# Kernel tuning notes

Hardware: AMD Instinct MI355X
Metric: run time of the kernel (lower is better)

Reference implementation:

```python
import jax, jax.numpy as jnp
import numpy as np

B, NC, CN, K, DN = 2, 256, 256, 16, 64
G, HM, HS, HMOD, MOD_OUT = 8, 128, 128, 64, 5


def setup_inputs() -> dict:
    rng = np.random.default_rng(0)
    # per-neuron top-K neighbors within cell, excluding self, sorted (matches torch buffer build)
    scores = rng.random((NC, CN, CN)).astype(np.float32)
    ii = np.arange(CN)
    scores[:, ii, ii] = -np.inf
    conn = np.argpartition(-scores, K, axis=-1)[..., :K]
    conn = np.sort(conn, axis=-1).astype(np.int32)  # [NC, CN, K]

    key = jax.random.key(0)
    ks = jax.random.split(key, 12)
    n = lambda k, s, sc=1.0: jax.random.normal(k, s, jnp.float32) * sc
    return {
        'h': n(ks[0], (B, NC, CN, DN), 0.01),
        'w_conn': n(ks[1], (B, NC, CN, K), 0.1),
        'cell_context': n(ks[2], (B, NC, DN), 0.1),
        'neuron_id': n(ks[3], (NC, CN, DN), 0.02),
        'msg_w1': n(ks[4], (G, HM, 3 * DN), 0.05), 'msg_b1': jnp.zeros((G, HM)),
        'msg_w2': n(ks[5], (G, DN, HM), 0.005), 'msg_b2': jnp.zeros((G, DN)),
        'state_w1': n(ks[6], (G, HS, 3 * DN), 0.05), 'state_b1': jnp.zeros((G, HS)),
        'state_w2': n(ks[7], (G, DN, HS), 0.005), 'state_b2': jnp.zeros((G, DN)),
        'mod_w1': n(ks[8], (NC, 2 * DN, HMOD), 0.05), 'mod_b1': jnp.zeros((NC, HMOD)),
        'mod_w2': n(ks[9], (NC, HMOD, MOD_OUT), 0.0005), 'mod_b2': jnp.zeros((NC, MOD_OUT)),
        'conn_idx': jnp.asarray(conn),
        'cell_to_group': (jnp.arange(NC) % G).astype(jnp.int32),
    }


def reference(h, w_conn, cell_context, neuron_id,
              msg_w1, msg_b1, msg_w2, msg_b2,
              state_w1, state_b1, state_w2, state_b2,
              mod_w1, mod_b1, mod_w2, mod_b2,
              conn_idx, cell_to_group):
    nc = h.shape[1]
    cell_ix = jnp.arange(nc)[:, None, None]
    # gather K-neighbor states per neuron: [B, NC, CN, K, DN]
    nb = jax.vmap(lambda hb: hb[cell_ix, conn_idx])(h)
    # connection-weighted aggregation
    agg = jnp.einsum('bnck,bnckd->bncd', w_conn, nb)

    g = cell_to_group  # [NC]
    # grouped message MLP (2-layer), per-cell weights gathered from group table
    mfeat = jnp.concatenate([h, agg, jnp.broadcast_to(neuron_id[None], h.shape)], axis=-1)
    mh = jax.nn.gelu(jnp.einsum('bncf,nhf->bnch', mfeat, msg_w1[g]) + msg_b1[g][None, :, None, :])
    msg = jnp.einsum('bnch,ndh->bncd', mh, msg_w2[g]) + msg_b2[g][None, :, None, :]

    # grouped state MLP, residual update on h
    ctx = jnp.broadcast_to(cell_context[:, :, None, :], h.shape)
    sfeat = jnp.concatenate([h, msg, ctx], axis=-1)
    sh = jax.nn.gelu(jnp.einsum('bncf,nhf->bnch', sfeat, state_w1[g]) + state_b1[g][None, :, None, :])
    h_new = h + jnp.einsum('bnch,ndh->bncd', sh, state_w2[g]) + state_b2[g][None, :, None, :]

    # per-cell modulation MLP on pooled stats (h_mean || msg_mean)
    pooled = jnp.concatenate([h_new.mean(axis=2), msg.mean(axis=2)], axis=-1)  # [B, NC, 2DN]
    ph = jax.nn.gelu(jnp.einsum('bnf,nfh->bnh', pooled, mod_w1) + mod_b1[None])
    mod = jnp.einsum('bnh,nho->bno', ph, mod_w2) + mod_b2[None]
    return h_new, msg, mod
```

## Files before the change

### kernel.cpp

```cpp
#include <hip/hip_runtime.h>

#define NC_  256
#define CN_  256
#define K_   16
#define DN_  64
#define G_   8
#define HM_  128
#define F3_  192

typedef unsigned short u16;
typedef short v8s __attribute__((ext_vector_type(8)));
typedef float v4f __attribute__((ext_vector_type(4)));


__device__ __forceinline__ u16 f2b(float f) {
    unsigned v; __builtin_memcpy(&v, &f, 4);
    v = v + 0x7fffu + ((v >> 16) & 1u);
    return (u16)(v >> 16);
}
__device__ __forceinline__ v8s cvt8(const float* p) {
    float4 a = *(const float4*)p, b = *(const float4*)(p + 4);
    v8s r;
    r[0] = (short)f2b(a.x); r[1] = (short)f2b(a.y); r[2] = (short)f2b(a.z); r[3] = (short)f2b(a.w);
    r[4] = (short)f2b(b.x); r[5] = (short)f2b(b.y); r[6] = (short)f2b(b.z); r[7] = (short)f2b(b.w);
    return r;
}
__device__ __forceinline__ float gelu_t(float x) {
    float u = x * x;
    float t = 1.5957691216057308f * x * __builtin_fmaf(0.044715f, u, 1.0f);
    float e = __expf(-t);
    return x * __builtin_amdgcn_rcpf(1.0f + e);
}

__global__ __launch_bounds__(256) void cvt_w(
    const float* __restrict__ mw1, const float* __restrict__ mw2,
    const float* __restrict__ sw1, const float* __restrict__ sw2,
    u16* __restrict__ dst)
{
    int e = (blockIdx.x * 256 + threadIdx.x) * 4;
    const float* s; int off;
    if      (e < 196608) { s = mw1; off = e; }
    else if (e < 262144) { s = mw2; off = e - 196608; }
    else if (e < 458752) { s = sw1; off = e - 262144; }
    else                 { s = sw2; off = e - 458752; }
    float4 v = *(const float4*)(s + off);
    ushort4 o4;
    o4.x = f2b(v.x); o4.y = f2b(v.y); o4.z = f2b(v.z); o4.w = f2b(v.w);
    *(ushort4*)(dst + e) = o4;
}

__global__ __launch_bounds__(256) void gth(
    const float* __restrict__ h, const float* __restrict__ wconn,
    const int* __restrict__ conn, float* __restrict__ outf)
{
    const int p     = blockIdx.x;
    const int bnc   = (p & 7) * 64 + (p >> 6);
    const int chunk = (p >> 3) & 7;
    const int wave  = threadIdx.x >> 6, lane = threadIdx.x & 63;
    const int r0    = chunk * 32 + wave * 8;
    const int n     = bnc & 255;
    const size_t hb = (size_t)bnc * 16384;
    const float* __restrict__ hp = h + hb;
    float* aggo = outf + (size_t)8388608 + hb;
    const int*   __restrict__ cp = conn  + n * 4096 + r0 * 16;
    const float* __restrict__ wp = wconn + (size_t)bnc * 4096 + (size_t)r0 * 16;
    int   ivA = cp[lane],      ivB = cp[64 + lane];
    float wvA = wp[lane],      wvB = wp[64 + lane];
#pragma unroll
    for (int i = 0; i < 8; ++i) {
        int   iv = (i < 4) ? ivA : ivB;
        float wv = (i < 4) ? wvA : wvB;
        float a0 = 0.0f, a1 = 0.0f;
#pragma unroll
        for (int k = 0; k < 16; k += 2) {
            const int l0 = (i & 3) * 16 + k;
            int   i0 = __builtin_amdgcn_readlane(iv, l0);
            int   i1 = __builtin_amdgcn_readlane(iv, l0 + 1);
            float w0 = __int_as_float(__builtin_amdgcn_readlane(__float_as_int(wv), l0));
            float w1 = __int_as_float(__builtin_amdgcn_readlane(__float_as_int(wv), l0 + 1));
            a0 = __builtin_fmaf(w0, hp[i0 * 64 + lane], a0);
            a1 = __builtin_fmaf(w1, hp[i1 * 64 + lane], a1);
        }
        aggo[(size_t)(r0 + i) * 64 + lane] = a0 + a1;
    }
}

__global__ __launch_bounds__(64, 3) void mg_main(
    const float* __restrict__ h,    const float* __restrict__ ctx,
    const float* __restrict__ nid,
    const u16* __restrict__ mw1b,   const float* __restrict__ mb1,
    const u16* __restrict__ mw2b,   const float* __restrict__ mb2,
    const u16* __restrict__ sw1b,   const float* __restrict__ sb1,
    const u16* __restrict__ sw2b,   const float* __restrict__ sb2,
    const int* __restrict__ c2g,
    float* __restrict__ outf,       float* __restrict__ partial)
{
    const int p     = blockIdx.x;
    const int bnc   = (p & 7) * 64 + (p >> 6);
    const int chunk = (p >> 3) & 7;
    const int r0    = chunk * 32;
    const int n     = bnc & 255;
    const int g     = c2g[n];
    const int lane  = threadIdx.x;
    const int q     = lane >> 4, ln = lane & 15;

    __shared__ u16 mh[32 * 138];
    __shared__ u16 am[32 * 74];

    const size_t hbase = (size_t)bnc * 16384;
    const size_t nbase = (size_t)n   * 16384;
    float* oH = outf + hbase;
    float* oM = outf + (size_t)8388608 + hbase;
    const size_t pbase = (size_t)(bnc * 8 + chunk) * 128;

    v8s hfr[2][2], gfr[2][2], nfr[2][2];
#pragma unroll
    for (int mi = 0; mi < 2; ++mi) {
        int c = r0 + mi * 16 + ln;
        hfr[mi][0] = cvt8(h   + hbase + (size_t)c * 64 +  0 + q * 8);
        hfr[mi][1] = cvt8(h   + hbase + (size_t)c * 64 + 32 + q * 8);
        gfr[mi][0] = cvt8(oM  + (size_t)c * 64 +  0 + q * 8);
        gfr[mi][1] = cvt8(oM  + (size_t)c * 64 + 32 + q * 8);
        nfr[mi][0] = cvt8(nid + nbase + (size_t)c * 64 +  0 + q * 8);
        nfr[mi][1] = cvt8(nid + nbase + (size_t)c * 64 + 32 + q * 8);
    }

    {
        v8s afr0[6] = {hfr[0][0], hfr[0][1], gfr[0][0], gfr[0][1], nfr[0][0], nfr[0][1]};
        v8s afr1[6] = {hfr[1][0], hfr[1][1], gfr[1][0], gfr[1][1], nfr[1][0], nfr[1][1]};
        float b1v[8];
#pragma unroll
        for (int nt = 0; nt < 8; ++nt) b1v[nt] = mb1[g * HM_ + nt * 16 + ln];
        const u16* w1g = mw1b + (size_t)g * HM_ * F3_;
#pragma unroll
        for (int nt = 0; nt < 8; ++nt) {
            v4f acc0 = {0,0,0,0}, acc1 = {0,0,0,0};
#pragma unroll
            for (int ks = 0; ks < 6; ++ks) {
                v8s bf = *(const v8s*)(w1g + (nt * 16 + ln) * F3_ + ks * 32 + q * 8);
                acc0 = __builtin_amdgcn_mfma_f32_16x16x32_bf16(afr0[ks], bf, acc0, 0, 0, 0);
                acc1 = __builtin_amdgcn_mfma_f32_16x16x32_bf16(afr1[ks], bf, acc1, 0, 0, 0);
            }
            int c0 = q * 4, c1 = 16 + q * 4;
#pragma unroll
            for (int r = 0; r < 4; ++r) {
                mh[(c0 + r) * 138 + nt * 16 + ln] = f2b(gelu_t(acc0[r] + b1v[nt]));
                mh[(c1 + r) * 138 + nt * 16 + ln] = f2b(gelu_t(acc1[r] + b1v[nt]));
            }
        }
    }

    {
        v8s afr[2][4];
#pragma unroll
        for (int mi = 0; mi < 2; ++mi) {
            int c = mi * 16 + ln;
#pragma unroll
            for (int ks = 0; ks < 4; ++ks)
                afr[mi][ks] = *(const v8s*)(mh + c * 138 + ks * 32 + q * 8);
        }
        const u16* w2g = mw2b + (size_t)g * DN_ * HM_;
        float mpart[4];
#pragma unroll
        for (int nt = 0; nt < 4; ++nt) {
            float bb = mb2[g * DN_ + nt * 16 + ln];
            v4f acc[2] = {{0,0,0,0},{0,0,0,0}};
#pragma unroll
            for (int ks = 0; ks < 4; ++ks) {
                v8s bf = *(const v8s*)(w2g + (nt * 16 + ln) * HM_ + ks * 32 + q * 8);
#pragma unroll
                for (int mi = 0; mi < 2; ++mi)
                    acc[mi] = __builtin_amdgcn_mfma_f32_16x16x32_bf16(afr[mi][ks], bf, acc[mi], 0, 0, 0);
            }
            float ms = 0.0f;
            int d = nt * 16 + ln;
#pragma unroll
            for (int mi = 0; mi < 2; ++mi) {
                int c = mi * 16 + q * 4;
#pragma unroll
                for (int r = 0; r < 4; ++r) {
                    float mv = acc[mi][r] + bb;
                    am[(c + r) * 74 + d] = f2b(mv);
                    oM[(size_t)(r0 + c + r) * 64 + d] = mv;
                    ms += mv;
                }
            }
            mpart[nt] = ms;
        }
#pragma unroll
        for (int nt = 0; nt < 4; ++nt) {
            float v = mpart[nt];
            v += __shfl_xor(v, 16);
            v += __shfl_xor(v, 32);
            if (q == 0) partial[pbase + 64 + nt * 16 + ln] = v * (1.0f / 256.0f);
        }
    }

    {
        v8s cfr0 = cvt8(ctx + (size_t)bnc * DN_ +  0 + q * 8);
        v8s cfr1 = cvt8(ctx + (size_t)bnc * DN_ + 32 + q * 8);
        v8s afr[2][4];
#pragma unroll
        for (int mi = 0; mi < 2; ++mi) {
            int c = mi * 16 + ln;
            afr[mi][0] = hfr[mi][0];
            afr[mi][1] = hfr[mi][1];
            afr[mi][2] = *(const v8s*)(am + c * 74 +  0 + q * 8);
            afr[mi][3] = *(const v8s*)(am + c * 74 + 32 + q * 8);
        }
        float b1v[8];
#pragma unroll
        for (int nt = 0; nt < 8; ++nt) b1v[nt] = sb1[g * HM_ + nt * 16 + ln];
        const u16* w1g = sw1b + (size_t)g * HM_ * F3_;
#pragma unroll
        for (int nt = 0; nt < 8; ++nt) {
            v4f acc[2] = {{0,0,0,0},{0,0,0,0}};
#pragma unroll
            for (int ks = 0; ks < 4; ++ks) {
                v8s bf = *(const v8s*)(w1g + (nt * 16 + ln) * F3_ + ks * 32 + q * 8);
#pragma unroll
                for (int mi = 0; mi < 2; ++mi)
                    acc[mi] = __builtin_amdgcn_mfma_f32_16x16x32_bf16(afr[mi][ks], bf, acc[mi], 0, 0, 0);
            }
#pragma unroll
            for (int ks = 4; ks < 6; ++ks) {
                v8s bf = *(const v8s*)(w1g + (nt * 16 + ln) * F3_ + ks * 32 + q * 8);
                v8s aa = (ks == 4) ? cfr0 : cfr1;
#pragma unroll
                for (int mi = 0; mi < 2; ++mi)
                    acc[mi] = __builtin_amdgcn_mfma_f32_16x16x32_bf16(aa, bf, acc[mi], 0, 0, 0);
            }
#pragma unroll
            for (int mi = 0; mi < 2; ++mi) {
                int c = mi * 16 + q * 4;
#pragma unroll
                for (int r = 0; r < 4; ++r)
                    mh[(c + r) * 138 + nt * 16 + ln] = f2b(gelu_t(acc[mi][r] + b1v[nt]));
            }
        }
    }

    {
        v8s afr[2][4];
#pragma unroll
        for (int mi = 0; mi < 2; ++mi) {
            int c = mi * 16 + ln;
#pragma unroll
            for (int ks = 0; ks < 4; ++ks)
                afr[mi][ks] = *(const v8s*)(mh + c * 138 + ks * 32 + q * 8);
        }
        const u16* w2g = sw2b + (size_t)g * DN_ * HM_;
        float hpart[4];
#pragma unroll
        for (int nt = 0; nt < 4; ++nt) {
            float bb = sb2[g * DN_ + nt * 16 + ln];
            v4f acc[2] = {{0,0,0,0},{0,0,0,0}};
#pragma unroll
            for (int ks = 0; ks < 4; ++ks) {
                v8s bf = *(const v8s*)(w2g + (nt * 16 + ln) * HM_ + ks * 32 + q * 8);
#pragma unroll
                for (int mi = 0; mi < 2; ++mi)
                    acc[mi] = __builtin_amdgcn_mfma_f32_16x16x32_bf16(afr[mi][ks], bf, acc[mi], 0, 0, 0);
            }
            float hs = 0.0f;
            int d = nt * 16 + ln;
#pragma unroll
            for (int mi = 0; mi < 2; ++mi) {
                int c = mi * 16 + q * 4;
#pragma unroll
                for (int r = 0; r < 4; ++r) {
                    float hv = h[hbase + (size_t)(r0 + c + r) * 64 + d];
                    float hn = hv + acc[mi][r] + bb;
                    oH[(size_t)(r0 + c + r) * 64 + d] = hn;
                    hs += hn;
                }
            }
            hpart[nt] = hs;
        }
#pragma unroll
        for (int nt = 0; nt < 4; ++nt) {
            float v = hpart[nt];
            v += __shfl_xor(v, 16);
            v += __shfl_xor(v, 32);
            if (q == 0) partial[pbase + nt * 16 + ln] = v * (1.0f / 256.0f);
        }
    }
}

__global__ __launch_bounds__(256) void mg_mod(
    const float* __restrict__ w1, const float* __restrict__ b1,
    const float* __restrict__ w2, const float* __restrict__ b2,
    const float* __restrict__ partial, float* __restrict__ outf)
{
    __shared__ float pool[128];
    __shared__ float ph4[4][64];
    const int bnc = blockIdx.x, n = bnc & 255, t = threadIdx.x;
    if (t < 128) {
        const float* pp = partial + (size_t)bnc * 1024 + t;
        float s = 0.0f;
#pragma unroll
        for (int j = 0; j < 8; ++j) s += pp[j * 128];
        pool[t] = s;
    }
    __syncthreads();
    {
        const int col = t & 63, fh = t >> 6;
        const float* w1p = w1 + ((size_t)n * 128 + fh * 32) * 64 + col;
        float acc = 0.0f;
#pragma unroll
        for (int i = 0; i < 32; ++i)
            acc = __builtin_fmaf(pool[fh * 32 + i], w1p[(size_t)i * 64], acc);
        ph4[fh][col] = acc;
    }
    __syncthreads();
    if (t < 64) {
        float a  = ph4[0][t] + ph4[1][t] + ph4[2][t] + ph4[3][t] + b1[n * 64 + t];
        float ph = gelu_t(a);
        float part5[5];
#pragma unroll
        for (int o = 0; o < 5; ++o) part5[o] = ph * w2[((size_t)n * 64 + t) * 5 + o];
#pragma unroll
        for (int off = 32; off > 0; off >>= 1)
#pragma unroll
            for (int o = 0; o < 5; ++o) part5[o] += __shfl_down(part5[o], off);
        if (t == 0) {
#pragma unroll
            for (int o = 0; o < 5; ++o)
                outf[(size_t)16777216 + bnc * 5 + o] = part5[o] + b2[n * 5 + o];
        }
    }
}

extern "C" void kernel_launch(void* const* d_in, const int* in_sizes, int n_in,
                              void* d_out, int out_size, void* d_ws, size_t ws_size,
                              hipStream_t stream) {
    const float* h     = (const float*)d_in[0];
    const float* wconn = (const float*)d_in[1];
    const float* ctx   = (const float*)d_in[2];
    const float* nid   = (const float*)d_in[3];
    const float* mw1   = (const float*)d_in[4];
    const float* mb1   = (const float*)d_in[5];
    const float* mw2   = (const float*)d_in[6];
    const float* mb2   = (const float*)d_in[7];
    const float* sw1   = (const float*)d_in[8];
    const float* sb1   = (const float*)d_in[9];
    const float* sw2   = (const float*)d_in[10];
    const float* sb2   = (const float*)d_in[11];
    const float* dw1   = (const float*)d_in[12];
    const float* db1   = (const float*)d_in[13];
    const float* dw2   = (const float*)d_in[14];
    const float* db2   = (const float*)d_in[15];
    const int* conn    = (const int*)d_in[16];
    const int* c2g     = (const int*)d_in[17];
    float* outf    = (float*)d_out;
    u16*   wb      = (u16*)d_ws;
    float* partial = (float*)((char*)d_ws + 1048576);

    cvt_w<<<512, 256, 0, stream>>>(mw1, mw2, sw1, sw2, wb);
    gth<<<4096, 256, 0, stream>>>(h, wconn, conn, outf);
    mg_main<<<4096, 64, 0, stream>>>(h, ctx, nid,
                                     wb,           mb1,
                                     wb + 196608,  mb2,
                                     wb + 262144,  sb1,
                                     wb + 458752,  sb2,
                                     c2g, outf, partial);
    mg_mod<<<512, 256, 0, stream>>>(dw1, db1, dw2, db2, partial, outf);
}
```

Before: 259.8 us.

## Stage per-cell h in LDS as bf16 for neighbor gather; raise mg_main occupancy

```diff
diff --git a/kernel.cpp b/kernel.cpp
--- a/kernel.cpp
+++ b/kernel.cpp
@@ -53,39 +53,54 @@
     const float* __restrict__ h, const float* __restrict__ wconn,
     const int* __restrict__ conn, float* __restrict__ outf)
 {
-    const int p     = blockIdx.x;
-    const int bnc   = (p & 7) * 64 + (p >> 6);
-    const int chunk = (p >> 3) & 7;
-    const int wave  = threadIdx.x >> 6, lane = threadIdx.x & 63;
-    const int r0    = chunk * 32 + wave * 8;
-    const int n     = bnc & 255;
+    __shared__ u16 hl[16384];
+    const int p    = blockIdx.x;
+    const int bnc  = (p & 7) * 64 + ((p >> 3) & 63);
+    const int half = p >> 9;
+    const int tid  = threadIdx.x;
+    const int wave = tid >> 6, lane = tid & 63;
+    const int r0   = half * 128 + wave * 32;
+    const int n    = bnc & 255;
     const size_t hb = (size_t)bnc * 16384;
-    const float* __restrict__ hp = h + hb;
+
+#pragma unroll
+    for (int i = 0; i < 16; ++i) {
+        float4 v = *(const float4*)(h + hb + tid * 4 + i * 1024);
+        ushort4 o;
+        o.x = f2b(v.x); o.y = f2b(v.y); o.z = f2b(v.z); o.w = f2b(v.w);
+        *(ushort4*)(hl + tid * 4 + i * 1024) = o;
+    }
+    __syncthreads();
+
     float* aggo = outf + (size_t)8388608 + hb;
     const int*   __restrict__ cp = conn  + n * 4096 + r0 * 16;
     const float* __restrict__ wp = wconn + (size_t)bnc * 4096 + (size_t)r0 * 16;
-    int   ivA = cp[lane],      ivB = cp[64 + lane];
-    float wvA = wp[lane],      wvB = wp[64 + lane];
-#pragma unroll
-    for (int i = 0; i < 8; ++i) {
-        int   iv = (i < 4) ? ivA : ivB;
-        float wv = (i < 4) ? wvA : wvB;
-        float a0 = 0.0f, a1 = 0.0f;
-#pragma unroll
-        for (int k = 0; k < 16; k += 2) {
-            const int l0 = (i & 3) * 16 + k;
-            int   i0 = __builtin_amdgcn_readlane(iv, l0);
-            int   i1 = __builtin_amdgcn_readlane(iv, l0 + 1);
-            float w0 = __int_as_float(__builtin_amdgcn_readlane(__float_as_int(wv), l0));
-            float w1 = __int_as_float(__builtin_amdgcn_readlane(__float_as_int(wv), l0 + 1));
-            a0 = __builtin_fmaf(w0, hp[i0 * 64 + lane], a0);
-            a1 = __builtin_fmaf(w1, hp[i1 * 64 + lane], a1);
-        }
-        aggo[(size_t)(r0 + i) * 64 + lane] = a0 + a1;
-    }
-}
-
-__global__ __launch_bounds__(64, 3) void mg_main(
+    int iv = cp[lane]; float wv = wp[lane];
+    for (int g4 = 0; g4 < 8; ++g4) {
+        int ivn = 0; float wvn = 0.0f;
+        if (g4 < 7) { ivn = cp[(g4 + 1) * 64 + lane]; wvn = wp[(g4 + 1) * 64 + lane]; }
+#pragma unroll
+        for (int r = 0; r < 4; ++r) {
+            float a0 = 0.0f, a1 = 0.0f;
+#pragma unroll
+            for (int k = 0; k < 16; k += 2) {
+                const int l0 = r * 16 + k;
+                int   i0 = __builtin_amdgcn_readlane(iv, l0);
+                int   i1 = __builtin_amdgcn_readlane(iv, l0 + 1);
+                float w0 = __int_as_float(__builtin_amdgcn_readlane(__float_as_int(wv), l0));
+                float w1 = __int_as_float(__builtin_amdgcn_readlane(__float_as_int(wv), l0 + 1));
+                unsigned h0 = (unsigned)hl[i0 * 64 + lane] << 16;
+                unsigned h1 = (unsigned)hl[i1 * 64 + lane] << 16;
+                a0 = __builtin_fmaf(w0, __uint_as_float(h0), a0);
+                a1 = __builtin_fmaf(w1, __uint_as_float(h1), a1);
+            }
+            aggo[(size_t)(r0 + g4 * 4 + r) * 64 + lane] = a0 + a1;
+        }
+        iv = ivn; wv = wvn;
+    }
+}
+
+__global__ __launch_bounds__(64, 4) void mg_main(
     const float* __restrict__ h,    const float* __restrict__ ctx,
     const float* __restrict__ nid,
     const u16* __restrict__ mw1b,   const float* __restrict__ mb1,
@@ -104,8 +119,7 @@
     const int lane  = threadIdx.x;
     const int q     = lane >> 4, ln = lane & 15;
 
-    __shared__ u16 mh[32 * 138];
-    __shared__ u16 am[32 * 74];
+    __shared__ u16 buf[32 * 138];
 
     const size_t hbase = (size_t)bnc * 16384;
     const size_t nbase = (size_t)n   * 16384;
@@ -144,8 +158,8 @@
             int c0 = q * 4, c1 = 16 + q * 4;
 #pragma unroll
             for (int r = 0; r < 4; ++r) {
-                mh[(c0 + r) * 138 + nt * 16 + ln] = f2b(gelu_t(acc0[r] + b1v[nt]));
-                mh[(c1 + r) * 138 + nt * 16 + ln] = f2b(gelu_t(acc1[r] + b1v[nt]));
+                buf[(c0 + r) * 138 + nt * 16 + ln] = f2b(gelu_t(acc0[r] + b1v[nt]));
+                buf[(c1 + r) * 138 + nt * 16 + ln] = f2b(gelu_t(acc1[r] + b1v[nt]));
             }
         }
     }
@@ -157,7 +171,7 @@
             int c = mi * 16 + ln;
 #pragma unroll
             for (int ks = 0; ks < 4; ++ks)
-                afr[mi][ks] = *(const v8s*)(mh + c * 138 + ks * 32 + q * 8);
+                afr[mi][ks] = *(const v8s*)(buf + c * 138 + ks * 32 + q * 8);
         }
         const u16* w2g = mw2b + (size_t)g * DN_ * HM_;
         float mpart[4];
@@ -180,7 +194,7 @@
 #pragma unroll
                 for (int r = 0; r < 4; ++r) {
                     float mv = acc[mi][r] + bb;
-                    am[(c + r) * 74 + d] = f2b(mv);
+                    buf[(c + r) * 138 + d] = f2b(mv);
                     oM[(size_t)(r0 + c + r) * 64 + d] = mv;
                     ms += mv;
                 }
@@ -205,8 +219,8 @@
             int c = mi * 16 + ln;
             afr[mi][0] = hfr[mi][0];
             afr[mi][1] = hfr[mi][1];
-            afr[mi][2] = *(const v8s*)(am + c * 74 +  0 + q * 8);
-            afr[mi][3] = *(const v8s*)(am + c * 74 + 32 + q * 8);
+            afr[mi][2] = *(const v8s*)(buf + c * 138 +  0 + q * 8);
+            afr[mi][3] = *(const v8s*)(buf + c * 138 + 32 + q * 8);
         }
         float b1v[8];
 #pragma unroll
@@ -235,7 +249,7 @@
                 int c = mi * 16 + q * 4;
 #pragma unroll
                 for (int r = 0; r < 4; ++r)
-                    mh[(c + r) * 138 + nt * 16 + ln] = f2b(gelu_t(acc[mi][r] + b1v[nt]));
+                    buf[(c + r) * 138 + nt * 16 + ln] = f2b(gelu_t(acc[mi][r] + b1v[nt]));
             }
         }
     }
@@ -247,7 +261,7 @@
             int c = mi * 16 + ln;
 #pragma unroll
             for (int ks = 0; ks < 4; ++ks)
-                afr[mi][ks] = *(const v8s*)(mh + c * 138 + ks * 32 + q * 8);
+                afr[mi][ks] = *(const v8s*)(buf + c * 138 + ks * 32 + q * 8);
         }
         const u16* w2g = sw2b + (size_t)g * DN_ * HM_;
         float hpart[4];
@@ -357,7 +371,7 @@
     float* partial = (float*)((char*)d_ws + 1048576);
 
     cvt_w<<<512, 256, 0, stream>>>(mw1, mw2, sw1, sw2, wb);
-    gth<<<4096, 256, 0, stream>>>(h, wconn, conn, outf);
+    gth<<<1024, 256, 0, stream>>>(h, wconn, conn, outf);
     mg_main<<<4096, 64, 0, stream>>>(h, ctx, nid,
                                      wb,           mb1,
                                      wb + 196608,  mb2,
```

Measured after the change: 243.2 us. -6.4%, faster.
